# Kernel tuning notes

Measured on AMD Instinct MI355X. Metric: run time of the kernel, lower is better.

## Reference

```python
import jax, jax.numpy as jnp
import numpy as np

B, T, S, F, D, M = 8, 8192, 8192, 64, 64, 128
EPS = 1e-9


def _draw_omega(n_omega, d_feature, rng):
    # Stacked orthogonal blocks scaled by sqrt(d_feature), as in the TF module.
    n_blocks = (n_omega + d_feature - 1) // d_feature + 1
    blocks = []
    for _ in range(n_blocks):
        g = rng.standard_normal((d_feature, d_feature)).astype(np.float32)
        q, _ = np.linalg.qr(g)
        blocks.append(q * np.sqrt(float(d_feature)))
    return jnp.asarray(np.concatenate(blocks, axis=0)[:n_omega])


def setup_inputs() -> dict:
    k0 = jax.random.key(0)
    kq, kv, kk = jax.random.split(k0, 3)
    query = jax.random.normal(kq, (B, T, F), dtype=jnp.float32)
    value = jax.random.normal(kv, (B, S, D), dtype=jnp.float32)
    key = jax.random.normal(kk, (B, S, F), dtype=jnp.float32)
    omega = _draw_omega(M, F, np.random.default_rng(0))  # (M, F)
    return {"query": query, "value": value, "key": key, "omega": omega}


def _phi(x, omega):
    # x: (B, L, F) -> (B, L, 2M) positive random features
    m = omega.shape[0]
    square_sum = jnp.sum(x * x, axis=-1, keepdims=True) / 2.0  # (B, L, 1)
    xw = jnp.einsum('blf,mf->blm', x, omega)                   # (B, L, M)
    unnorm = jnp.exp(jnp.concatenate([xw, -xw], axis=-1) - square_sum) + EPS
    return unnorm / jnp.sqrt(2.0 * m)


def reference(query, value, key, omega):
    q = _phi(query, omega)  # (B, T, 2M)
    k = _phi(key, omega)    # (B, S, 2M)
    ones = jnp.ones(value.shape[:-1] + (1,), dtype=value.dtype)
    v1 = jnp.concatenate([value, ones], axis=-1)               # (B, S, D+1)
    kv = jnp.einsum('bsm,bsd->bmd', k, v1)                     # (B, 2M, D+1)
    qkv = jnp.einsum('btm,bmd->btd', q, kv)                    # (B, T, D+1)
    normalizer = qkv[:, :, -1:]
    return qkv[:, :, :-1] / normalizer
```

## Files before the change

### kernel.cpp

```cpp
#include <hip/hip_runtime.h>


constexpr int NB = 8;
constexpr int NT = 8192;
constexpr float EPSF = 1e-9f;
constexpr float SCALE = 0.0625f;

typedef short s8v __attribute__((ext_vector_type(8)));
typedef short s4v __attribute__((ext_vector_type(4)));
typedef float f4v __attribute__((ext_vector_type(4)));

__device__ inline f4v mfma16(s8v a, s8v b, f4v c) {
  return __builtin_amdgcn_mfma_f32_16x16x32_bf16(a, b, c, 0, 0, 0);
}

__device__ inline short bf16_rne(float f) {
  unsigned u = __builtin_bit_cast(unsigned, f);
  u += 0x7fffu + ((u >> 16) & 1u);
  return (short)(u >> 16);
}
__device__ inline float bf16_to_f(short h) {
  unsigned u = ((unsigned)(unsigned short)h) << 16;
  return __builtin_bit_cast(float, u);
}
__device__ inline unsigned pack2(short lo, short hi) {
  return (unsigned)(unsigned short)lo | ((unsigned)(unsigned short)hi << 16);
}

__global__ void setup_omega(const float* __restrict__ omega,
                            short* __restrict__ oh, short* __restrict__ ol) {
  int i = blockIdx.x * 256 + threadIdx.x;
  if (i >= 128 * 64) return;
  float w = omega[i];
  short h = bf16_rne(w);
  oh[i] = h;
  ol[i] = bf16_rne(w - bf16_to_f(h));
}

struct PhiRows {
  s8v ah0, al0, ah1, al1;
  float ssr[4];
  float ss;
};

__device__ inline void split8(f4v a, f4v b, s8v& h, s8v& l) {
  float v[8] = {a.x, a.y, a.z, a.w, b.x, b.y, b.z, b.w};
#pragma unroll
  for (int j = 0; j < 8; ++j) {
    short hh = bf16_rne(v[j]);
    h[j] = hh;
    l[j] = bf16_rne(v[j] - bf16_to_f(hh));
  }
}

__device__ inline void load_phi_rows(const float* __restrict__ xrow_base, int lane, PhiRows& P) {
  const int r = lane & 15, q = lane >> 4;
  const float* p = xrow_base + r * 64 + q * 8;
  f4v u0 = *(const f4v*)(p);
  f4v u1 = *(const f4v*)(p + 4);
  f4v u2 = *(const f4v*)(p + 32);
  f4v u3 = *(const f4v*)(p + 36);
  float ss = u0.x * u0.x + u0.y * u0.y + u0.z * u0.z + u0.w * u0.w
           + u1.x * u1.x + u1.y * u1.y + u1.z * u1.z + u1.w * u1.w
           + u2.x * u2.x + u2.y * u2.y + u2.z * u2.z + u2.w * u2.w
           + u3.x * u3.x + u3.y * u3.y + u3.z * u3.z + u3.w * u3.w;
  ss += __shfl_xor(ss, 16, 64);
  ss += __shfl_xor(ss, 32, 64);
  ss *= 0.5f;
  P.ss = ss;
#pragma unroll
  for (int reg = 0; reg < 4; ++reg) P.ssr[reg] = __shfl(ss, q * 4 + reg, 64);
  split8(u0, u1, P.ah0, P.al0);
  split8(u2, u3, P.ah1, P.al1);
}

__device__ inline f4v phi_xw_tile(const PhiRows& P, const short* __restrict__ oh,
                                  const short* __restrict__ ol, int f0, int lane) {
  const int fr = f0 + (lane & 15);
  const int q = lane >> 4;
  s8v bh0 = *(const s8v*)(oh + fr * 64 + q * 8);
  s8v bh1 = *(const s8v*)(oh + fr * 64 + 32 + q * 8);
  s8v bl0 = *(const s8v*)(ol + fr * 64 + q * 8);
  s8v bl1 = *(const s8v*)(ol + fr * 64 + 32 + q * 8);
  f4v c = {0.f, 0.f, 0.f, 0.f};
  c = mfma16(P.ah0, bh0, c);
  c = mfma16(P.ah1, bh1, c);
  c = mfma16(P.al0, bh0, c);
  c = mfma16(P.al1, bh1, c);
  c = mfma16(P.ah0, bl0, c);
  c = mfma16(P.ah1, bl1, c);
  return c;
}

__device__ inline f4v phi_xw_tile_T(const PhiRows& P, const short* __restrict__ oh,
                                    const short* __restrict__ ol, int f0, int lane) {
  const int fr = f0 + (lane & 15);
  const int q = lane >> 4;
  s8v ah0 = *(const s8v*)(oh + fr * 64 + q * 8);
  s8v ah1 = *(const s8v*)(oh + fr * 64 + 32 + q * 8);
  s8v al0 = *(const s8v*)(ol + fr * 64 + q * 8);
  s8v al1 = *(const s8v*)(ol + fr * 64 + 32 + q * 8);
  f4v c = {0.f, 0.f, 0.f, 0.f};
  c = mfma16(ah0, P.ah0, c);
  c = mfma16(ah1, P.ah1, c);
  c = mfma16(al0, P.ah0, c);
  c = mfma16(al1, P.ah1, c);
  c = mfma16(ah0, P.al0, c);
  c = mfma16(ah1, P.al1, c);
  return c;
}

__device__ inline s8v bfrag_shuffle(unsigned g0d0, unsigned g0d1,
                                    unsigned g1d0, unsigned g1d1, int lane) {
  const int sb = ((lane & 16) ? 32 : 0) | (lane & 15);
  int a0 = __shfl((int)g0d0, sb, 64);
  int a1 = __shfl((int)g0d1, sb, 64);
  int a2 = __shfl((int)g0d0, sb + 16, 64);
  int a3 = __shfl((int)g0d1, sb + 16, 64);
  int b0 = __shfl((int)g1d0, sb, 64);
  int b1 = __shfl((int)g1d1, sb, 64);
  int b2 = __shfl((int)g1d0, sb + 16, 64);
  int b3 = __shfl((int)g1d1, sb + 16, 64);
  const bool hi = lane >= 32;
  int4 r;
  r.x = hi ? b0 : a0;
  r.y = hi ? b1 : a1;
  r.z = hi ? b2 : a2;
  r.w = hi ? b3 : a3;
  return __builtin_bit_cast(s8v, r);
}

constexpr int KF_P = 72;
constexpr int PART_SZ = 65 * 256;

__global__ __launch_bounds__(256, 2) void kv_fused(
    const float* __restrict__ key, const float* __restrict__ value,
    const short* __restrict__ oh, const short* __restrict__ ol,
    short* __restrict__ partial, float* __restrict__ kvacc, int use_partial) {
  __shared__ short kft[256 * KF_P];
  __shared__ short v1t[80 * KF_P];
  const int tid = threadIdx.x, lane = tid & 63, w = tid >> 6;
  const int b = blockIdx.x >> 6;
  const int s0 = (blockIdx.x & 63) * 128;
  const int q = lane >> 4, r15 = lane & 15;

  for (int i = tid; i < 15 * KF_P; i += 256) v1t[65 * KF_P + i] = 0;

  f4v acc[4][5];
#pragma unroll
  for (int j = 0; j < 4; ++j)
#pragma unroll
    for (int n = 0; n < 5; ++n) acc[j][n] = f4v{0.f, 0.f, 0.f, 0.f};

  for (int sc = 0; sc < 2; ++sc) {
    const int sbase = s0 + sc * 64;
    __syncthreads();
    {
      const float* vb = value + ((size_t)b * NT + sbase) * 64;
#pragma unroll
      for (int i = 0; i < 4; ++i) {
        int e4 = tid + i * 256;
        f4v v4 = ((const f4v*)vb)[e4];
        int s = e4 >> 4, d0 = (e4 & 15) * 4;
        v1t[(d0 + 0) * KF_P + s] = bf16_rne(v4.x);
        v1t[(d0 + 1) * KF_P + s] = bf16_rne(v4.y);
        v1t[(d0 + 2) * KF_P + s] = bf16_rne(v4.z);
        v1t[(d0 + 3) * KF_P + s] = bf16_rne(v4.w);
      }
      if (tid < 64) v1t[64 * KF_P + tid] = (short)0x3F80;
    }
    {
      PhiRows P;
      load_phi_rows(key + ((size_t)b * NT + sbase + w * 16) * 64, lane, P);
#pragma unroll
      for (int ft = 0; ft < 8; ++ft) {
        f4v c = phi_xw_tile(P, oh, ol, ft * 16, lane);
        s4v pk, nk;
#pragma unroll
        for (int reg = 0; reg < 4; ++reg) {
          float xw = c[reg];
          pk[reg] = bf16_rne((__expf(xw - P.ssr[reg]) + EPSF) * SCALE);
          nk[reg] = bf16_rne((__expf(-xw - P.ssr[reg]) + EPSF) * SCALE);
        }
        const int scol = w * 16 + q * 4;
        *(s4v*)(kft + (ft * 16 + r15) * KF_P + scol) = pk;
        *(s4v*)(kft + (128 + ft * 16 + r15) * KF_P + scol) = nk;
      }
    }
    __syncthreads();
#pragma unroll
    for (int ks = 0; ks < 2; ++ks) {
      s8v bf[5];
#pragma unroll
      for (int n = 0; n < 5; ++n)
        bf[n] = *(const s8v*)(v1t + (n * 16 + r15) * KF_P + ks * 32 + q * 8);
#pragma unroll
      for (int j = 0; j < 4; ++j) {
        s8v a = *(const s8v*)(kft + (w * 64 + j * 16 + r15) * KF_P + ks * 32 + q * 8);
#pragma unroll
        for (int n = 0; n < 5; ++n) acc[j][n] = mfma16(a, bf[n], acc[j][n]);
      }
    }
  }
  if (use_partial) {
    short* pb = partial + (size_t)blockIdx.x * PART_SZ;
#pragma unroll
    for (int j = 0; j < 4; ++j) {
      int m = w * 64 + j * 16 + q * 4;
#pragma unroll
      for (int n = 0; n < 4; ++n) {
        int d = n * 16 + r15;
        s4v pk;
#pragma unroll
        for (int reg = 0; reg < 4; ++reg) pk[reg] = bf16_rne(acc[j][n][reg]);
        *(s4v*)(pb + d * 256 + m) = pk;
      }
      if (r15 == 0) {
        s4v pk;
#pragma unroll
        for (int reg = 0; reg < 4; ++reg) pk[reg] = bf16_rne(acc[j][4][reg]);
        *(s4v*)(pb + 64 * 256 + m) = pk;
      }
    }
  } else {
    float* pb = kvacc + (size_t)b * PART_SZ;
#pragma unroll
    for (int j = 0; j < 4; ++j) {
      int m = w * 64 + j * 16 + q * 4;
#pragma unroll
      for (int n = 0; n < 4; ++n) {
        int d = n * 16 + r15;
#pragma unroll
        for (int reg = 0; reg < 4; ++reg) atomicAdd(pb + d * 256 + m + reg, acc[j][n][reg]);
      }
      if (r15 == 0)
#pragma unroll
        for (int reg = 0; reg < 4; ++reg) atomicAdd(pb + 64 * 256 + m + reg, acc[j][4][reg]);
    }
  }
}

__global__ __launch_bounds__(256) void kv_finalize(
    const short* __restrict__ partial, const float* __restrict__ kvacc,
    short* __restrict__ kvfrag, int use_partial) {
  int i = blockIdx.x * 256 + threadIdx.x;
  int b = i / 20480;
  int rem = i - b * 20480;
  int d = rem >> 8;
  int m = rem & 255;
  float s = 0.f;
  if (d < 65) {
    if (use_partial) {
      const short* p = partial + (size_t)(b * 64) * PART_SZ + d * 256 + m;
#pragma unroll 8
      for (int c = 0; c < 64; ++c) s += bf16_to_f(p[(size_t)c * PART_SZ]);
    } else {
      s = kvacc[(size_t)b * PART_SZ + d * 256 + m];
    }
  }
  int ks = m >> 5, qq = (m >> 3) & 3, j = m & 7;
  int n = d >> 4, r = d & 15;
  int lane = qq * 16 + r;
  kvfrag[(((size_t)b * 40 + ks * 5 + n) * 64 + lane) * 8 + j] = bf16_rne(s);
}

__global__ __launch_bounds__(256, 4) void qkv_fused(
    const float* __restrict__ query, const short* __restrict__ oh,
    const short* __restrict__ ol, const short* __restrict__ kvfrag,
    float* __restrict__ out) {
  __shared__ __align__(16) float stg[4][16 * 68];
  const int tid = threadIdx.x, lane = tid & 63, w = tid >> 6;
  const int b = blockIdx.x >> 7;
  const int t0 = (blockIdx.x & 127) * 64;
  const int q = lane >> 4, r15 = lane & 15;

  PhiRows P;
  load_phi_rows(query + ((size_t)b * NT + t0 + w * 16) * 64, lane, P);

  f4v acc[5];
#pragma unroll
  for (int n = 0; n < 5; ++n) acc[n] = f4v{0.f, 0.f, 0.f, 0.f};
  const short* kvb = kvfrag + (size_t)b * 40 * 512;

#pragma unroll
  for (int kp = 0; kp < 4; ++kp) {
    f4v c0 = phi_xw_tile_T(P, oh, ol, kp * 32, lane);
    f4v c1 = phi_xw_tile_T(P, oh, ol, kp * 32 + 16, lane);
    short p0[4], n0[4], p1[4], n1[4];
#pragma unroll
    for (int reg = 0; reg < 4; ++reg) {
      float x0 = c0[reg], x1 = c1[reg];
      p0[reg] = bf16_rne((__expf(x0 - P.ss) + EPSF) * SCALE);
      n0[reg] = bf16_rne((__expf(-x0 - P.ss) + EPSF) * SCALE);
      p1[reg] = bf16_rne((__expf(x1 - P.ss) + EPSF) * SCALE);
      n1[reg] = bf16_rne((__expf(-x1 - P.ss) + EPSF) * SCALE);
    }
    {
      s8v aP = bfrag_shuffle(pack2(p0[0], p0[1]), pack2(p0[2], p0[3]),
                             pack2(p1[0], p1[1]), pack2(p1[2], p1[3]), lane);
#pragma unroll
      for (int n = 0; n < 5; ++n) {
        s8v bf = *(const s8v*)(kvb + ((size_t)(kp * 5 + n)) * 512 + lane * 8);
        acc[n] = mfma16(aP, bf, acc[n]);
      }
    }
    {
      s8v aN = bfrag_shuffle(pack2(n0[0], n0[1]), pack2(n0[2], n0[3]),
                             pack2(n1[0], n1[1]), pack2(n1[2], n1[3]), lane);
#pragma unroll
      for (int n = 0; n < 5; ++n) {
        s8v bf = *(const s8v*)(kvb + ((size_t)((kp + 4) * 5 + n)) * 512 + lane * 8);
        acc[n] = mfma16(aN, bf, acc[n]);
      }
    }
  }
  float den_r[4];
#pragma unroll
  for (int reg = 0; reg < 4; ++reg) den_r[reg] = __shfl(acc[4][reg], lane & 48, 64);
  float* sg = stg[w];
#pragma unroll
  for (int n = 0; n < 4; ++n)
#pragma unroll
    for (int reg = 0; reg < 4; ++reg) {
      int row = q * 4 + reg;
      int col = n * 16 + r15;
      sg[row * 68 + col] = acc[n][reg] / den_r[reg];
    }
  float* ob = out + ((size_t)b * NT + t0 + w * 16) * 64;
#pragma unroll
  for (int rr = 0; rr < 4; ++rr) {
    int row = rr * 4 + q;
    int c4 = r15 * 4;
    *(f4v*)(ob + row * 64 + c4) = *(const f4v*)(sg + row * 68 + c4);
  }
}

extern "C" void kernel_launch(void* const* d_in, const int* in_sizes, int n_in,
                              void* d_out, int out_size, void* d_ws, size_t ws_size,
                              hipStream_t stream) {
  const float* query = (const float*)d_in[0];
  const float* value = (const float*)d_in[1];
  const float* key   = (const float*)d_in[2];
  const float* omega = (const float*)d_in[3];
  float* out = (float*)d_out;

  char* ws = (char*)d_ws;
  short* oh = (short*)ws;
  short* ol = (short*)(ws + 16384);
  short* kvfrag = (short*)(ws + 32768);
  short* partial = (short*)(ws + 360448);
  float* kvacc = (float*)(ws + 360448);
  const size_t need_full = 360448 + (size_t)512 * PART_SZ * 2;
  const int use_partial = (ws_size >= need_full) ? 1 : 0;

  setup_omega<<<32, 256, 0, stream>>>(omega, oh, ol);
  if (!use_partial) {
    hipMemsetAsync(kvacc, 0, (size_t)8 * PART_SZ * 4, stream);
  }
  kv_fused<<<512, 256, 0, stream>>>(key, value, oh, ol, partial, kvacc, use_partial);
  kv_finalize<<<640, 256, 0, stream>>>(partial, kvacc, kvfrag, use_partial);
  qkv_fused<<<1024, 256, 0, stream>>>(query, oh, ol, kvfrag, out);
}
```

Before: 143.9 us.

## Merge four kernel launches into two cooperative kernels with grid syncs

Folds the omega split and the KV partial accumulation into one cooperative kernel, and the partial reduction and query pass into a second, each separated by a grid-wide sync instead of a kernel boundary. The aim is to remove launch gaps and tail idle time between the four small kernels. Occupancy and CU counts are queried on every call, and the old path is kept as a fallback when residency is too low or the cooperative launch fails. Grid sync cost and the per-call host queries may offset the launch savings.

```diff
diff --git a/kernel.cpp b/kernel.cpp
--- a/kernel.cpp
+++ b/kernel.cpp
@@ -1,4 +1,7 @@
 #include <hip/hip_runtime.h>
+#include <hip/hip_cooperative_groups.h>
+
+namespace cg = cooperative_groups;
 
 
 constexpr int NB = 8;
@@ -27,14 +30,20 @@
   return (unsigned)(unsigned short)lo | ((unsigned)(unsigned short)hi << 16);
 }
 
+__device__ inline void omega_split_item(const float* __restrict__ omega,
+                                        short* __restrict__ oh, short* __restrict__ ol,
+                                        int i) {
+  float w = omega[i];
+  short h = bf16_rne(w);
+  oh[i] = h;
+  ol[i] = bf16_rne(w - bf16_to_f(h));
+}
+
 __global__ void setup_omega(const float* __restrict__ omega,
                             short* __restrict__ oh, short* __restrict__ ol) {
   int i = blockIdx.x * 256 + threadIdx.x;
   if (i >= 128 * 64) return;
-  float w = omega[i];
-  short h = bf16_rne(w);
-  oh[i] = h;
-  ol[i] = bf16_rne(w - bf16_to_f(h));
+  omega_split_item(omega, oh, ol, i);
 }
 
 struct PhiRows {
@@ -133,15 +142,18 @@
 constexpr int KF_P = 72;
 constexpr int PART_SZ = 65 * 256;
 
-__global__ __launch_bounds__(256, 2) void kv_fused(
-    const float* __restrict__ key, const float* __restrict__ value,
-    const short* __restrict__ oh, const short* __restrict__ ol,
-    short* __restrict__ partial, float* __restrict__ kvacc, int use_partial) {
-  __shared__ short kft[256 * KF_P];
-  __shared__ short v1t[80 * KF_P];
-  const int tid = threadIdx.x, lane = tid & 63, w = tid >> 6;
-  const int b = blockIdx.x >> 6;
-  const int s0 = (blockIdx.x & 63) * 128;
+template <bool USE_PARTIAL>
+__device__ inline void kv_body(int it, int tid,
+                               const float* __restrict__ key,
+                               const float* __restrict__ value,
+                               const short* __restrict__ oh,
+                               const short* __restrict__ ol,
+                               short* __restrict__ partial,
+                               float* __restrict__ kvacc,
+                               short* kft, short* v1t) {
+  const int lane = tid & 63, w = tid >> 6;
+  const int b = it >> 6;
+  const int s0 = (it & 63) * 128;
   const int q = lane >> 4, r15 = lane & 15;
 
   for (int i = tid; i < 15 * KF_P; i += 256) v1t[65 * KF_P + i] = 0;
@@ -202,8 +214,8 @@
       }
     }
   }
-  if (use_partial) {
-    short* pb = partial + (size_t)blockIdx.x * PART_SZ;
+  if (USE_PARTIAL) {
+    short* pb = partial + (size_t)it * PART_SZ;
 #pragma unroll
     for (int j = 0; j < 4; ++j) {
       int m = w * 64 + j * 16 + q * 4;
@@ -240,23 +252,17 @@
   }
 }
 
-__global__ __launch_bounds__(256) void kv_finalize(
-    const short* __restrict__ partial, const float* __restrict__ kvacc,
-    short* __restrict__ kvfrag, int use_partial) {
-  int i = blockIdx.x * 256 + threadIdx.x;
+__device__ inline void finalize_item(int i, const short* __restrict__ partial,
+                                     short* __restrict__ kvfrag) {
   int b = i / 20480;
   int rem = i - b * 20480;
   int d = rem >> 8;
   int m = rem & 255;
   float s = 0.f;
   if (d < 65) {
-    if (use_partial) {
-      const short* p = partial + (size_t)(b * 64) * PART_SZ + d * 256 + m;
+    const short* p = partial + (size_t)(b * 64) * PART_SZ + d * 256 + m;
 #pragma unroll 8
-      for (int c = 0; c < 64; ++c) s += bf16_to_f(p[(size_t)c * PART_SZ]);
-    } else {
-      s = kvacc[(size_t)b * PART_SZ + d * 256 + m];
-    }
+    for (int c = 0; c < 64; ++c) s += bf16_to_f(p[(size_t)c * PART_SZ]);
   }
   int ks = m >> 5, qq = (m >> 3) & 3, j = m & 7;
   int n = d >> 4, r = d & 15;
@@ -264,14 +270,15 @@
   kvfrag[(((size_t)b * 40 + ks * 5 + n) * 64 + lane) * 8 + j] = bf16_rne(s);
 }
 
-__global__ __launch_bounds__(256, 4) void qkv_fused(
-    const float* __restrict__ query, const short* __restrict__ oh,
-    const short* __restrict__ ol, const short* __restrict__ kvfrag,
-    float* __restrict__ out) {
-  __shared__ __align__(16) float stg[4][16 * 68];
-  const int tid = threadIdx.x, lane = tid & 63, w = tid >> 6;
-  const int b = blockIdx.x >> 7;
-  const int t0 = (blockIdx.x & 127) * 64;
+__device__ inline void qkv_body(int it, int tid,
+                                const float* __restrict__ query,
+                                const short* __restrict__ oh,
+                                const short* __restrict__ ol,
+                                const short* __restrict__ kvfrag,
+                                float* __restrict__ out, float* stg4) {
+  const int lane = tid & 63, w = tid >> 6;
+  const int b = it >> 7;
+  const int t0 = (it & 127) * 64;
   const int q = lane >> 4, r15 = lane & 15;
 
   PhiRows P;
@@ -317,7 +324,7 @@
   float den_r[4];
 #pragma unroll
   for (int reg = 0; reg < 4; ++reg) den_r[reg] = __shfl(acc[4][reg], lane & 48, 64);
-  float* sg = stg[w];
+  float* sg = stg4 + w * (16 * 68);
 #pragma unroll
   for (int n = 0; n < 4; ++n)
 #pragma unroll
@@ -333,6 +340,74 @@
     int c4 = r15 * 4;
     *(f4v*)(ob + row * 64 + c4) = *(const f4v*)(sg + row * 68 + c4);
   }
+}
+
+__global__ __launch_bounds__(256, 2) void coop_k1(
+    const float* __restrict__ omega, const float* __restrict__ key,
+    const float* __restrict__ value, short* __restrict__ oh,
+    short* __restrict__ ol, short* __restrict__ partial) {
+  __shared__ short kft[256 * KF_P];
+  __shared__ short v1t[80 * KF_P];
+  const int tid = threadIdx.x;
+  for (int i = blockIdx.x * 256 + tid; i < 128 * 64; i += gridDim.x * 256)
+    omega_split_item(omega, oh, ol, i);
+  __threadfence();
+  cg::this_grid().sync();
+  for (int it = blockIdx.x; it < 512; it += gridDim.x)
+    kv_body<true>(it, tid, key, value, oh, ol, partial, nullptr, kft, v1t);
+}
+
+__global__ __launch_bounds__(256, 4) void coop_k2(
+    const float* __restrict__ query, const short* __restrict__ oh,
+    const short* __restrict__ ol, const short* __restrict__ partial,
+    short* __restrict__ kvfrag, float* __restrict__ out) {
+  __shared__ __align__(16) float stg[4 * 16 * 68];
+  const int tid = threadIdx.x;
+  for (int i = blockIdx.x * 256 + tid; i < 163840; i += gridDim.x * 256)
+    finalize_item(i, partial, kvfrag);
+  __threadfence();
+  cg::this_grid().sync();
+  for (int it = blockIdx.x; it < 1024; it += gridDim.x)
+    qkv_body(it, tid, query, oh, ol, kvfrag, out, stg);
+}
+
+__global__ __launch_bounds__(256, 2) void kv_fused(
+    const float* __restrict__ key, const float* __restrict__ value,
+    const short* __restrict__ oh, const short* __restrict__ ol,
+    short* __restrict__ partial, float* __restrict__ kvacc, int use_partial) {
+  __shared__ short kft[256 * KF_P];
+  __shared__ short v1t[80 * KF_P];
+  if (use_partial)
+    kv_body<true>(blockIdx.x, threadIdx.x, key, value, oh, ol, partial, kvacc, kft, v1t);
+  else
+    kv_body<false>(blockIdx.x, threadIdx.x, key, value, oh, ol, partial, kvacc, kft, v1t);
+}
+
+__global__ __launch_bounds__(256) void kv_finalize(
+    const short* __restrict__ partial, const float* __restrict__ kvacc,
+    short* __restrict__ kvfrag, int use_partial) {
+  int i = blockIdx.x * 256 + threadIdx.x;
+  if (use_partial) {
+    finalize_item(i, partial, kvfrag);
+  } else {
+    int b = i / 20480;
+    int rem = i - b * 20480;
+    int d = rem >> 8;
+    int m = rem & 255;
+    float s = (d < 65) ? kvacc[(size_t)b * PART_SZ + d * 256 + m] : 0.f;
+    int ks = m >> 5, qq = (m >> 3) & 3, j = m & 7;
+    int n = d >> 4, r = d & 15;
+    int lane = qq * 16 + r;
+    kvfrag[(((size_t)b * 40 + ks * 5 + n) * 64 + lane) * 8 + j] = bf16_rne(s);
+  }
+}
+
+__global__ __launch_bounds__(256, 4) void qkv_fused(
+    const float* __restrict__ query, const short* __restrict__ oh,
+    const short* __restrict__ ol, const short* __restrict__ kvfrag,
+    float* __restrict__ out) {
+  __shared__ __align__(16) float stg[4 * 16 * 68];
+  qkv_body(blockIdx.x, threadIdx.x, query, oh, ol, kvfrag, out, stg);
 }
 
 extern "C" void kernel_launch(void* const* d_in, const int* in_sizes, int n_in,
@@ -353,11 +428,35 @@
   const size_t need_full = 360448 + (size_t)512 * PART_SZ * 2;
   const int use_partial = (ws_size >= need_full) ? 1 : 0;
 
-  setup_omega<<<32, 256, 0, stream>>>(omega, oh, ol);
-  if (!use_partial) {
-    hipMemsetAsync(kvacc, 0, (size_t)8 * PART_SZ * 4, stream);
-  }
-  kv_fused<<<512, 256, 0, stream>>>(key, value, oh, ol, partial, kvacc, use_partial);
-  kv_finalize<<<640, 256, 0, stream>>>(partial, kvacc, kvfrag, use_partial);
-  qkv_fused<<<1024, 256, 0, stream>>>(query, oh, ol, kvfrag, out);
-}
+  bool did_k1 = false, did_k2 = false;
+  if (use_partial) {
+    int dev = 0;
+    hipGetDevice(&dev);
+    int num_cu = 0;
+    hipDeviceGetAttribute(&num_cu, hipDeviceAttributeMultiprocessorCount, dev);
+    int mb1 = 0, mb2 = 0;
+    hipOccupancyMaxActiveBlocksPerMultiprocessor(&mb1, (const void*)coop_k1, 256, 0);
+    hipOccupancyMaxActiveBlocksPerMultiprocessor(&mb2, (const void*)coop_k2, 256, 0);
+    if ((long)mb1 * num_cu >= 512) {
+      void* a1[] = {(void*)&omega, (void*)&key, (void*)&value,
+                    (void*)&oh, (void*)&ol, (void*)&partial};
+      did_k1 = (hipLaunchCooperativeKernel((void*)coop_k1, dim3(512), dim3(256),
+                                           a1, 0, stream) == hipSuccess);
+    }
+    if (did_k1 && (long)mb2 * num_cu >= 1024) {
+      void* a2[] = {(void*)&query, (void*)&oh, (void*)&ol,
+                    (void*)&partial, (void*)&kvfrag, (void*)&out};
+      did_k2 = (hipLaunchCooperativeKernel((void*)coop_k2, dim3(1024), dim3(256),
+                                           a2, 0, stream) == hipSuccess);
+    }
+  }
+  if (!did_k1) {
+    setup_omega<<<32, 256, 0, stream>>>(omega, oh, ol);
+    if (!use_partial) hipMemsetAsync(kvacc, 0, (size_t)8 * PART_SZ * 4, stream);
+    kv_fused<<<512, 256, 0, stream>>>(key, value, oh, ol, partial, kvacc, use_partial);
+  }
+  if (!did_k2) {
+    kv_finalize<<<640, 256, 0, stream>>>(partial, kvacc, kvfrag, use_partial);
+    qkv_fused<<<1024, 256, 0, stream>>>(query, oh, ol, kvfrag, out);
+  }
+}
```

Result: slower. 174.3 us (+21.1%).
